# Optimization experiments

Measured on AMD Instinct MI355X. Metric: run time of the kernel, lower is better.

The kernel has to match this reference:

```python
import jax, jax.numpy as jnp
import numpy as np

N, M, E = 20000, 5000, 320000   # nodes, hyperedges, incidence edges
HEADS, OUT, EDIM = 4, 32, 32
NEG_SLOPE = 0.2


def setup_inputs() -> dict:
    key = jax.random.key(0)
    ks = jax.random.split(key, 7)
    feat = jax.random.normal(ks[0], (N, HEADS * OUT), jnp.float32)
    edge_feat = jax.random.normal(ks[1], (E, EDIM), jnp.float32)
    H = jax.random.uniform(ks[2], (N, M), jnp.float32)
    attn_l = jax.random.normal(ks[3], (1, HEADS, OUT), jnp.float32)
    attn_m = jax.random.normal(ks[4], (1, HEADS, EDIM), jnp.float32)
    src = jax.random.randint(ks[5], (E,), 0, N, jnp.int32)
    dst = jax.random.randint(ks[6], (E,), 0, M, jnp.int32)
    return dict(feat=feat, edge_feat=edge_feat, H=H,
                attn_l=attn_l, attn_m=attn_m, src=src, dst=dst)


def _segment_softmax(e, seg, num):
    # numerically stable softmax over edges grouped by destination segment
    emax = jax.ops.segment_max(e, seg, num_segments=num)
    emax = jnp.where(jnp.isfinite(emax), emax, 0.0)  # guard empty segments
    ex = jnp.exp(e - emax[seg])
    den = jax.ops.segment_sum(ex, seg, num_segments=num)
    return ex / den[seg]


def reference(feat, edge_feat, H, attn_l, attn_m, src, dst):
    feat_src = feat.reshape(-1, HEADS, OUT)                 # [N,h,d]
    el = (feat_src * attn_l).sum(-1)                        # [N,h]
    em = (edge_feat[:, None, :] * attn_m).sum(-1)           # [E,h]
    e = el[src] + em                                        # [E,h]
    e = jnp.where(e > 0, e, NEG_SLOPE * e)                  # LeakyReLU
    a = _segment_softmax(e, dst, M)                         # edge softmax per dst
    msg = feat_src[src] * a[..., None]                      # [E,h,d]
    agg = jax.ops.segment_sum(msg, dst, num_segments=M)     # [M,h,d]
    rst = jnp.einsum('nm,mdk->ndk', H, agg)                 # [N,h,d]
    return rst.reshape(rst.shape[0], -1)
```

## Files before the change

kernel.cpp:

```cpp
#include <hip/hip_runtime.h>

#define NN 20000
#define MM 5000
#define EE 320000
#define FD 128
#define KD 5000
#define K2 5120
#define NEG 0.2f
#define BK 128
#define BUFB 65536
#define BOFF 32768
#define NKT 40
#define SPLITK 4
#define KTPS 10
#define PS4 640000

typedef __attribute__((ext_vector_type(4))) float f32x4;
typedef __attribute__((ext_vector_type(8))) short short8;

__device__ __forceinline__ unsigned int f2bf(float x){
  unsigned int u = __float_as_uint(x);
  return (u + 0x7fffu + ((u >> 16) & 1u)) >> 16;
}
__device__ __forceinline__ unsigned int cvtpk(float lo, float hi){
  unsigned int r;
  asm volatile("v_cvt_pk_bf16_f32 %0, %1, %2" : "=v"(r) : "v"(lo), "v"(hi));
  return r;
}
__device__ __forceinline__ void dma16(const void* g, void* l){
  __builtin_amdgcn_global_load_lds(
      (const __attribute__((address_space(1))) void*)g,
      (__attribute__((address_space(3))) void*)l, 16, 0, 0);
}

__global__ __launch_bounds__(256) void k_el(const float* __restrict__ feat,
                                            const float* __restrict__ attn_l,
                                            float* __restrict__ el){
  int t = threadIdx.x;
  int node = blockIdx.x*4 + (t>>6);
  int l = t & 63;
  float2 f = ((const float2*)feat)[(size_t)node*64 + l];
  float p = f.x*attn_l[2*l] + f.y*attn_l[2*l+1];
  p += __shfl_xor(p,1); p += __shfl_xor(p,2); p += __shfl_xor(p,4); p += __shfl_xor(p,8);
  if ((l&15)==0) el[node*4 + (l>>4)] = p;
}

__global__ __launch_bounds__(256) void k_feat16(const float4* __restrict__ feat,
                                                uint4* __restrict__ fb){
  int i = blockIdx.x*256 + threadIdx.x;
  float4 a = feat[2*i], b = feat[2*i+1];
  uint4 r;
  r.x = cvtpk(a.x,a.y); r.y = cvtpk(a.z,a.w);
  r.z = cvtpk(b.x,b.y); r.w = cvtpk(b.z,b.w);
  fb[i] = r;
}

__global__ __launch_bounds__(256) void k_edge(const float* __restrict__ edge_feat,
                                              const float* __restrict__ attn_m,
                                              const float* __restrict__ el,
                                              const int* __restrict__ src,
                                              const int* __restrict__ dst,
                                              int* __restrict__ counts,
                                              float4* __restrict__ e4){
  __shared__ float am[128];
  int t = threadIdx.x;
  if (t < 128) am[t] = attn_m[t];
  __syncthreads();
  int e = blockIdx.x*16 + (t>>4);
  int c = t & 15;
  float2 f = ((const float2*)edge_feat)[(size_t)e*16 + c];
  float p0 = f.x*am[0*32+2*c] + f.y*am[0*32+2*c+1];
  float p1 = f.x*am[1*32+2*c] + f.y*am[1*32+2*c+1];
  float p2 = f.x*am[2*32+2*c] + f.y*am[2*32+2*c+1];
  float p3 = f.x*am[3*32+2*c] + f.y*am[3*32+2*c+1];
  #pragma unroll
  for (int s=1; s<16; s<<=1){
    p0 += __shfl_xor(p0,s); p1 += __shfl_xor(p1,s);
    p2 += __shfl_xor(p2,s); p3 += __shfl_xor(p3,s);
  }
  if (c==0){
    float4 ev = ((const float4*)el)[src[e]];
    float4 r;
    float v;
    v = ev.x + p0; r.x = v > 0.f ? v : NEG*v;
    v = ev.y + p1; r.y = v > 0.f ? v : NEG*v;
    v = ev.z + p2; r.z = v > 0.f ? v : NEG*v;
    v = ev.w + p3; r.w = v > 0.f ? v : NEG*v;
    e4[e] = r;
    atomicAdd(&counts[dst[e]], 1);
  }
}

__global__ __launch_bounds__(256) void k_scan(const int* __restrict__ counts,
                                              int* __restrict__ offsets){
  __shared__ int sc[256];
  int t = threadIdx.x;
  int loc[20];
  int sum = 0;
  #pragma unroll
  for (int j=0;j<20;j++){
    int idx = t*20 + j;
    int v = (idx < MM) ? counts[idx] : 0;
    loc[j] = sum; sum += v;
  }
  sc[t] = sum; __syncthreads();
  for (int s=1; s<256; s<<=1){
    int v = 0;
    if (t >= s) v = sc[t-s];
    __syncthreads();
    if (t >= s) sc[t] += v;
    __syncthreads();
  }
  int base = sc[t] - sum;
  #pragma unroll
  for (int j=0;j<20;j++){
    int idx = t*20 + j;
    if (idx < MM) offsets[idx] = base + loc[j];
  }
  if (t == 250) offsets[MM] = base;
}

__global__ __launch_bounds__(256) void k_scatter(const int* __restrict__ dst,
                                                 const int* __restrict__ src,
                                                 const float4* __restrict__ e4,
                                                 const int* __restrict__ offsets,
                                                 int* __restrict__ cursor,
                                                 int* __restrict__ src_s,
                                                 float4* __restrict__ e4_s){
  int e = blockIdx.x*256 + threadIdx.x;
  if (e < EE){
    int d = dst[e];
    int pos = offsets[d] + atomicAdd(&cursor[d], 1);
    src_s[pos] = src[e];
    e4_s[pos] = e4[e];
  }
}

__global__ __launch_bounds__(256) void k_agg(const float4* __restrict__ e4_s,
                                             const int* __restrict__ src_s,
                                             const unsigned int* __restrict__ fb,
                                             const int* __restrict__ offsets,
                                             unsigned short* __restrict__ aggT){
  int m = blockIdx.x;
  int t = threadIdx.x;
  if (m < (K2 - KD) && t < FD) aggT[(size_t)t*K2 + KD + m] = 0;
  int beg = offsets[m], end = offsets[m+1];
  int cnt = end - beg;
  if (cnt == 0){
    if (t < FD) aggT[(size_t)t*K2 + m] = 0;
    return;
  }
  __shared__ float accs[4][FD];
  __shared__ float dens[4][4];
  int w = t>>6, l = t&63, h = l>>4;
  float accx=0.f, accy=0.f, den=0.f;
  int i = w;
  #pragma unroll 1
  for (; i+4 < cnt; i += 8){
    float4 ev0 = e4_s[beg+i];
    float4 ev1 = e4_s[beg+i+4];
    int s0 = src_s[beg+i];
    int s1 = src_s[beg+i+4];
    unsigned int v0 = fb[(size_t)s0*64 + l];
    unsigned int v1 = fb[(size_t)s1*64 + l];
    float eh0 = (h==0)?ev0.x:((h==1)?ev0.y:((h==2)?ev0.z:ev0.w));
    float eh1 = (h==0)?ev1.x:((h==1)?ev1.y:((h==2)?ev1.z:ev1.w));
    float p0 = __expf(eh0 - 32.0f);
    float p1 = __expf(eh1 - 32.0f);
    accx += p0*__uint_as_float(v0<<16) + p1*__uint_as_float(v1<<16);
    accy += p0*__uint_as_float(v0&0xffff0000u) + p1*__uint_as_float(v1&0xffff0000u);
    den  += p0 + p1;
  }
  if (i < cnt){
    float4 ev = e4_s[beg+i];
    int s0 = src_s[beg+i];
    unsigned int v = fb[(size_t)s0*64 + l];
    float eh = (h==0)?ev.x:((h==1)?ev.y:((h==2)?ev.z:ev.w));
    float p = __expf(eh - 32.0f);
    accx += p*__uint_as_float(v<<16);
    accy += p*__uint_as_float(v&0xffff0000u);
    den  += p;
  }
  accs[w][2*l]   = accx;
  accs[w][2*l+1] = accy;
  if ((l&15)==0) dens[w][h] = den;
  __syncthreads();
  if (t < FD){
    float s = accs[0][t]+accs[1][t]+accs[2][t]+accs[3][t];
    float dn = dens[0][t>>5]+dens[1][t>>5]+dens[2][t>>5]+dens[3][t>>5];
    aggT[(size_t)t*K2 + m] = (unsigned short)f2bf(s/dn);
  }
}

__global__ __launch_bounds__(512, 2) void k_gemm(const float* __restrict__ H,
                                                 const unsigned short* __restrict__ aggT,
                                                 float* __restrict__ part){
  __shared__ char lds[2*BUFB];
  int t = threadIdx.x;
  int row0 = blockIdx.x * 64;
  int kt0 = blockIdx.y * KTPS;

  int w8 = t>>6, l = t&63;
  const size_t AMAX = (size_t)NN*KD - 4;

  int wr = (w8>>2)*32, wc = (w8&3)*32;
  int rl = l&15, kg = l>>4;
  int arowA = (wr+rl)*512;
  int arowB = (wr+16+rl)*512;
  int bcol0 = BOFF + (wc+ 0+rl)*256;
  int bcol1 = BOFF + (wc+16+rl)*256;

  f32x4 acc00={0,0,0,0}, acc01={0,0,0,0};
  f32x4 acc10={0,0,0,0}, acc11={0,0,0,0};

#define STAGE(KT, BUF)                                                        \
  { size_t kb_ = (size_t)(KT)*BK;                                             \
    _Pragma("unroll")                                                         \
    for (int j=0;j<4;j++){                \
      int r_ = row0 + w8*8 + j*2 + (l>>5);                                    \
      if (r_ > NN-1) r_ = NN-1;                                               \
      size_t s_ = (size_t)r_*KD + (size_t)((l&31) ^ (r_&15))*4 + kb_;         \
      if (s_ > AMAX) s_ = AMAX;                                               \
      dma16(H + s_, (BUF) + (w8*8 + j*2)*512);                                \
    }                                                                         \
    _Pragma("unroll")                                                         \
    for (int j=0;j<4;j++){                \
      int c_ = w8*16 + j*4 + (l>>4);                                          \
      size_t s_ = (size_t)c_*K2 + (size_t)((l&15) ^ (c_&15))*8 + kb_;         \
      dma16(aggT + s_, (BUF) + BOFF + (w8*16 + j*4)*256);                     \
    }                                                                         \
  }

#define COMP_KK(R_, KK)                                                       \
  { int gA0 = (KK)*8 + kg*2;                                                  \
    int sA0 = ((gA0  ) ^ rl) << 4;                                            \
    int sA1 = ((gA0+1) ^ rl) << 4;                                            \
    f32x4 x0_ = *(const f32x4*)(R_ + arowA + sA0);                            \
    f32x4 x1_ = *(const f32x4*)(R_ + arowA + sA1);                            \
    f32x4 y0_ = *(const f32x4*)(R_ + arowB + sA0);                            \
    f32x4 y1_ = *(const f32x4*)(R_ + arowB + sA1);                            \
    int sB_ = (((KK)*4 + kg) ^ rl) << 4;                                      \
    short8 b0_ = *(const short8*)(R_ + bcol0 + sB_);                          \
    short8 b1_ = *(const short8*)(R_ + bcol1 + sB_);                          \
    uint4 ua_, ub_;                                                           \
    ua_.x = cvtpk(x0_[0],x0_[1]); ua_.y = cvtpk(x0_[2],x0_[3]);               \
    ua_.z = cvtpk(x1_[0],x1_[1]); ua_.w = cvtpk(x1_[2],x1_[3]);               \
    ub_.x = cvtpk(y0_[0],y0_[1]); ub_.y = cvtpk(y0_[2],y0_[3]);               \
    ub_.z = cvtpk(y1_[0],y1_[1]); ub_.w = cvtpk(y1_[2],y1_[3]);               \
    short8 a0_ = *(short8*)&ua_;                                              \
    short8 a1_ = *(short8*)&ub_;                                              \
    acc00 = __builtin_amdgcn_mfma_f32_16x16x32_bf16(a0_,b0_,acc00,0,0,0);     \
    acc01 = __builtin_amdgcn_mfma_f32_16x16x32_bf16(a0_,b1_,acc01,0,0,0);     \
    acc10 = __builtin_amdgcn_mfma_f32_16x16x32_bf16(a1_,b0_,acc10,0,0,0);     \
    acc11 = __builtin_amdgcn_mfma_f32_16x16x32_bf16(a1_,b1_,acc11,0,0,0);     \
  }

  STAGE(kt0,   lds)
  STAGE(kt0+1, lds + BUFB)

  int pr = 0;
  for (int tt = 0; tt < KTPS; ++tt){
    if (tt+1 < KTPS) { asm volatile("s_waitcnt vmcnt(8)" ::: "memory"); }
    else             { asm volatile("s_waitcnt vmcnt(0)" ::: "memory"); }
    __builtin_amdgcn_s_barrier();
    { const char* R_ = lds + pr*BUFB;
      COMP_KK(R_, 0)
      COMP_KK(R_, 1)
      COMP_KK(R_, 2)
      COMP_KK(R_, 3)
    }
    __builtin_amdgcn_s_barrier();
    __builtin_amdgcn_sched_barrier(0);
    if (tt+2 < KTPS) STAGE(kt0+tt+2, lds + pr*BUFB)
    pr ^= 1;
  }
#undef STAGE
#undef COMP_KK

  float* pout = part + (size_t)blockIdx.y*NN*FD;
#define STORE(ACC, FR, FN)                                                    \
  { _Pragma("unroll")                                                         \
    for (int q=0;q<4;q++){                                                    \
      int r = row0 + wr + (FR)*16 + kg*4 + q;                                 \
      if (r < NN) pout[(size_t)r*FD + wc + (FN)*16 + rl] = ACC[q];            \
    } }
  STORE(acc00,0,0) STORE(acc01,0,1)
  STORE(acc10,1,0) STORE(acc11,1,1)
#undef STORE
}

__global__ __launch_bounds__(256) void k_reduce(const float4* __restrict__ part,
                                                float4* __restrict__ out){
  int i = blockIdx.x*256 + threadIdx.x;
  float4 a = part[i];
  float4 b = part[i + 1*PS4];
  float4 c = part[i + 2*PS4];
  float4 d = part[i + 3*PS4];
  float4 r;
  r.x = (a.x+b.x)+(c.x+d.x);
  r.y = (a.y+b.y)+(c.y+d.y);
  r.z = (a.z+b.z)+(c.z+d.z);
  r.w = (a.w+b.w)+(c.w+d.w);
  out[i] = r;
}

extern "C" void kernel_launch(void* const* d_in, const int* in_sizes, int n_in,
                              void* d_out, int out_size, void* d_ws, size_t ws_size,
                              hipStream_t stream) {
  const float* feat      = (const float*)d_in[0];
  const float* edge_feat = (const float*)d_in[1];
  const float* H         = (const float*)d_in[2];
  const float* attn_l    = (const float*)d_in[3];
  const float* attn_m    = (const float*)d_in[4];
  const int*   src       = (const int*)d_in[5];
  const int*   dst       = (const int*)d_in[6];
  float* out = (float*)d_out;

  char* w = (char*)d_ws;
  float*          el       = (float*)(w + 0);
  unsigned short* aggT     = (unsigned short*)(w + 0);
  float4*         e4       = (float4*)(w + 1310720);
  int*            counts   = (int*)(w + 6430720);
  int*            cursor   = (int*)(w + 6451200);
  int*            offsets  = (int*)(w + 6471680);
  int*            src_s    = (int*)(w + 6492160);
  float4*         e4_s     = (float4*)(w + 7772160);
  unsigned int*   fb       = (unsigned int*)(w + 12892160);
  float*          part     = (float*)(w + 18012160);

  hipMemsetAsync(counts, 0, 2*20480, stream);

  k_feat16 <<<1250,   256, 0, stream>>>((const float4*)feat, (uint4*)fb);
  k_el     <<<NN/4,   256, 0, stream>>>(feat, attn_l, el);
  k_edge   <<<EE/16,  256, 0, stream>>>(edge_feat, attn_m, el, src, dst, counts, e4);
  k_scan   <<<1,      256, 0, stream>>>(counts, offsets);
  k_scatter<<<EE/256, 256, 0, stream>>>(dst, src, e4, offsets, cursor, src_s, e4_s);
  k_agg    <<<MM,     256, 0, stream>>>(e4_s, src_s, fb, offsets, aggT);
  k_gemm   <<<dim3((NN+63)/64, SPLITK), 512, 0, stream>>>(H, aggT, part);
  k_reduce <<<PS4/256, 256, 0, stream>>>((const float4*)part, (float4*)out);
}
```

Before: 216.9 us.

## Fuse preprocessing kernels and replace split-K partial buffer with atomic accumulation

Merges the bf16 feature conversion into the attention-logit kernel, so feat is read from memory once. Edge scoring is moved after the count/scan step so scores are written straight into CSR order, which removes the separate scatter pass and the intermediate e4 buffer. The split-K GEMM now adds its partial results into the zeroed output with float atomics instead of writing four partial slabs that a reduce kernel sums. In exchange it adds an output memset, an extra pass over dst for counting, atomic contention on the output, and a nondeterministic summation order.

```diff
diff --git a/kernel.cpp b/kernel.cpp
--- a/kernel.cpp
+++ b/kernel.cpp
@@ -13,7 +13,6 @@
 #define NKT 40
 #define SPLITK 4
 #define KTPS 10
-#define PS4 640000
 
 typedef __attribute__((ext_vector_type(4))) float f32x4;
 typedef __attribute__((ext_vector_type(8))) short short8;
@@ -33,35 +32,64 @@
       (__attribute__((address_space(3))) void*)l, 16, 0, 0);
 }
 
-__global__ __launch_bounds__(256) void k_el(const float* __restrict__ feat,
-                                            const float* __restrict__ attn_l,
-                                            float* __restrict__ el){
+__global__ __launch_bounds__(256) void k_prep(const float* __restrict__ feat,
+                                              const float* __restrict__ attn_l,
+                                              float* __restrict__ el,
+                                              unsigned int* __restrict__ fb){
   int t = threadIdx.x;
   int node = blockIdx.x*4 + (t>>6);
   int l = t & 63;
   float2 f = ((const float2*)feat)[(size_t)node*64 + l];
+  fb[(size_t)node*64 + l] = cvtpk(f.x, f.y);
   float p = f.x*attn_l[2*l] + f.y*attn_l[2*l+1];
   p += __shfl_xor(p,1); p += __shfl_xor(p,2); p += __shfl_xor(p,4); p += __shfl_xor(p,8);
   if ((l&15)==0) el[node*4 + (l>>4)] = p;
 }
 
-__global__ __launch_bounds__(256) void k_feat16(const float4* __restrict__ feat,
-                                                uint4* __restrict__ fb){
-  int i = blockIdx.x*256 + threadIdx.x;
-  float4 a = feat[2*i], b = feat[2*i+1];
-  uint4 r;
-  r.x = cvtpk(a.x,a.y); r.y = cvtpk(a.z,a.w);
-  r.z = cvtpk(b.x,b.y); r.w = cvtpk(b.z,b.w);
-  fb[i] = r;
-}
-
-__global__ __launch_bounds__(256) void k_edge(const float* __restrict__ edge_feat,
-                                              const float* __restrict__ attn_m,
-                                              const float* __restrict__ el,
-                                              const int* __restrict__ src,
-                                              const int* __restrict__ dst,
-                                              int* __restrict__ counts,
-                                              float4* __restrict__ e4){
+__global__ __launch_bounds__(256) void k_count(const int* __restrict__ dst,
+                                               int* __restrict__ counts){
+  int e = blockIdx.x*256 + threadIdx.x;
+  if (e < EE) atomicAdd(&counts[dst[e]], 1);
+}
+
+__global__ __launch_bounds__(256) void k_scan(const int* __restrict__ counts,
+                                              int* __restrict__ offsets){
+  __shared__ int sc[256];
+  int t = threadIdx.x;
+  int loc[20];
+  int sum = 0;
+  #pragma unroll
+  for (int j=0;j<20;j++){
+    int idx = t*20 + j;
+    int v = (idx < MM) ? counts[idx] : 0;
+    loc[j] = sum; sum += v;
+  }
+  sc[t] = sum; __syncthreads();
+  for (int s=1; s<256; s<<=1){
+    int v = 0;
+    if (t >= s) v = sc[t-s];
+    __syncthreads();
+    if (t >= s) sc[t] += v;
+    __syncthreads();
+  }
+  int base = sc[t] - sum;
+  #pragma unroll
+  for (int j=0;j<20;j++){
+    int idx = t*20 + j;
+    if (idx < MM) offsets[idx] = base + loc[j];
+  }
+  if (t == 250) offsets[MM] = base;
+}
+
+__global__ __launch_bounds__(256) void k_edge_sc(const float* __restrict__ edge_feat,
+                                                 const float* __restrict__ attn_m,
+                                                 const float* __restrict__ el,
+                                                 const int* __restrict__ src,
+                                                 const int* __restrict__ dst,
+                                                 const int* __restrict__ offsets,
+                                                 int* __restrict__ cursor,
+                                                 float4* __restrict__ e4_s,
+                                                 int* __restrict__ src_s){
   __shared__ float am[128];
   int t = threadIdx.x;
   if (t < 128) am[t] = attn_m[t];
@@ -86,53 +114,10 @@
     v = ev.y + p1; r.y = v > 0.f ? v : NEG*v;
     v = ev.z + p2; r.z = v > 0.f ? v : NEG*v;
     v = ev.w + p3; r.w = v > 0.f ? v : NEG*v;
-    e4[e] = r;
-    atomicAdd(&counts[dst[e]], 1);
-  }
-}
-
-__global__ __launch_bounds__(256) void k_scan(const int* __restrict__ counts,
-                                              int* __restrict__ offsets){
-  __shared__ int sc[256];
-  int t = threadIdx.x;
-  int loc[20];
-  int sum = 0;
-  #pragma unroll
-  for (int j=0;j<20;j++){
-    int idx = t*20 + j;
-    int v = (idx < MM) ? counts[idx] : 0;
-    loc[j] = sum; sum += v;
-  }
-  sc[t] = sum; __syncthreads();
-  for (int s=1; s<256; s<<=1){
-    int v = 0;
-    if (t >= s) v = sc[t-s];
-    __syncthreads();
-    if (t >= s) sc[t] += v;
-    __syncthreads();
-  }
-  int base = sc[t] - sum;
-  #pragma unroll
-  for (int j=0;j<20;j++){
-    int idx = t*20 + j;
-    if (idx < MM) offsets[idx] = base + loc[j];
-  }
-  if (t == 250) offsets[MM] = base;
-}
-
-__global__ __launch_bounds__(256) void k_scatter(const int* __restrict__ dst,
-                                                 const int* __restrict__ src,
-                                                 const float4* __restrict__ e4,
-                                                 const int* __restrict__ offsets,
-                                                 int* __restrict__ cursor,
-                                                 int* __restrict__ src_s,
-                                                 float4* __restrict__ e4_s){
-  int e = blockIdx.x*256 + threadIdx.x;
-  if (e < EE){
     int d = dst[e];
     int pos = offsets[d] + atomicAdd(&cursor[d], 1);
+    e4_s[pos] = r;
     src_s[pos] = src[e];
-    e4_s[pos] = e4[e];
   }
 }
 
@@ -194,7 +179,7 @@
 
 __global__ __launch_bounds__(512, 2) void k_gemm(const float* __restrict__ H,
                                                  const unsigned short* __restrict__ aggT,
-                                                 float* __restrict__ part){
+                                                 float* __restrict__ out){
   __shared__ char lds[2*BUFB];
   int t = threadIdx.x;
   int row0 = blockIdx.x * 64;
@@ -277,31 +262,15 @@
 #undef STAGE
 #undef COMP_KK
 
-  float* pout = part + (size_t)blockIdx.y*NN*FD;
 #define STORE(ACC, FR, FN)                                                    \
   { _Pragma("unroll")                                                         \
     for (int q=0;q<4;q++){                                                    \
       int r = row0 + wr + (FR)*16 + kg*4 + q;                                 \
-      if (r < NN) pout[(size_t)r*FD + wc + (FN)*16 + rl] = ACC[q];            \
+      if (r < NN) atomicAdd(&out[(size_t)r*FD + wc + (FN)*16 + rl], ACC[q]);  \
     } }
   STORE(acc00,0,0) STORE(acc01,0,1)
   STORE(acc10,1,0) STORE(acc11,1,1)
 #undef STORE
-}
-
-__global__ __launch_bounds__(256) void k_reduce(const float4* __restrict__ part,
-                                                float4* __restrict__ out){
-  int i = blockIdx.x*256 + threadIdx.x;
-  float4 a = part[i];
-  float4 b = part[i + 1*PS4];
-  float4 c = part[i + 2*PS4];
-  float4 d = part[i + 3*PS4];
-  float4 r;
-  r.x = (a.x+b.x)+(c.x+d.x);
-  r.y = (a.y+b.y)+(c.y+d.y);
-  r.z = (a.z+b.z)+(c.z+d.z);
-  r.w = (a.w+b.w)+(c.w+d.w);
-  out[i] = r;
 }
 
 extern "C" void kernel_launch(void* const* d_in, const int* in_sizes, int n_in,
@@ -319,23 +288,21 @@
   char* w = (char*)d_ws;
   float*          el       = (float*)(w + 0);
   unsigned short* aggT     = (unsigned short*)(w + 0);
-  float4*         e4       = (float4*)(w + 1310720);
-  int*            counts   = (int*)(w + 6430720);
-  int*            cursor   = (int*)(w + 6451200);
-  int*            offsets  = (int*)(w + 6471680);
-  int*            src_s    = (int*)(w + 6492160);
-  float4*         e4_s     = (float4*)(w + 7772160);
-  unsigned int*   fb       = (unsigned int*)(w + 12892160);
-  float*          part     = (float*)(w + 18012160);
+  int*            counts   = (int*)(w + 1310720);
+  int*            cursor   = (int*)(w + 1331200);
+  int*            offsets  = (int*)(w + 1351680);
+  int*            src_s    = (int*)(w + 1372160);
+  float4*         e4_s     = (float4*)(w + 2652160);
+  unsigned int*   fb       = (unsigned int*)(w + 7772160);
 
   hipMemsetAsync(counts, 0, 2*20480, stream);
-
-  k_feat16 <<<1250,   256, 0, stream>>>((const float4*)feat, (uint4*)fb);
-  k_el     <<<NN/4,   256, 0, stream>>>(feat, attn_l, el);
-  k_edge   <<<EE/16,  256, 0, stream>>>(edge_feat, attn_m, el, src, dst, counts, e4);
+  hipMemsetAsync(out, 0, (size_t)out_size*4, stream);
+
+  k_prep   <<<NN/4,   256, 0, stream>>>(feat, attn_l, el, fb);
+  k_count  <<<EE/256, 256, 0, stream>>>(dst, counts);
   k_scan   <<<1,      256, 0, stream>>>(counts, offsets);
-  k_scatter<<<EE/256, 256, 0, stream>>>(dst, src, e4, offsets, cursor, src_s, e4_s);
+  k_edge_sc<<<EE/16,  256, 0, stream>>>(edge_feat, attn_m, el, src, dst,
+                                        offsets, cursor, e4_s, src_s);
   k_agg    <<<MM,     256, 0, stream>>>(e4_s, src_s, fb, offsets, aggT);
-  k_gemm   <<<dim3((NN+63)/64, SPLITK), 512, 0, stream>>>(H, aggT, part);
-  k_reduce <<<PS4/256, 256, 0, stream>>>((const float4*)part, (float4*)out);
-}
+  k_gemm   <<<dim3((NN+63)/64, SPLITK), 512, 0, stream>>>(H, aggT, out);
+}
```

Result: no change. 215.5 us (-0.7%).
